# Performance work log

Hardware: AMD Instinct MI355X
Metric: run time of the kernel (lower is better)

Reference implementation:

```python
import jax, jax.numpy as jnp
import numpy as np
import math

N_PATHS = 2048
N_STEPS = 512
N_FWD = 40
N_FACTORS = 3
H = 0.1
ALPHA = H - 0.5            # fBM kernel exponent
BETA_SABR = 0.5
SHIFT = 0.02
DT = 1.0 / N_STEPS
GAMMA_CONST = math.gamma(H + 0.5)
BETA_DECAY = 0.05


def setup_inputs() -> dict:
    key = jax.random.key(0)
    tenors = np.linspace(0.0, 10.0, N_FWD + 1)
    T = tenors[:-1]
    tau = np.diff(tenors).astype(np.float32)
    F0 = np.full(N_FWD, 0.02, dtype=np.float32)
    # alphas = base normal vols / |F0+shift|^beta  (as in __init__)
    base_vols = np.full(N_FWD, 0.006)
    eta_F0 = np.abs(F0 + SHIFT) ** BETA_SABR
    alphas = (base_vols / eta_F0).astype(np.float32)
    rhos = np.full(N_FWD, -0.3, dtype=np.float32)
    nus = np.full(N_FWD, 0.5, dtype=np.float32)
    # PCA loadings from exponential spatial correlation (as in __init__)
    corr = np.exp(-BETA_DECAY * np.abs(T[:, None] - T[None, :]))
    evals, evecs = np.linalg.eigh(corr)
    idx = np.argsort(evals)[::-1][:N_FACTORS]
    L = evecs[:, idx] * np.sqrt(np.clip(evals[idx], 0.0, None))[None, :]
    L = L / np.sqrt((L ** 2).sum(axis=1, keepdims=True))
    Lam = np.triu(L @ L.T, 1).astype(np.float32)
    # Brownian increments, pre-scaled by sqrt(dt) (replaces Sobol+icdf draw)
    dz = jax.random.normal(key, (N_PATHS, N_STEPS, N_FACTORS + 1), dtype=jnp.float32) * float(np.sqrt(DT))
    return {
        "dz_all": dz,
        "F0": jnp.asarray(F0),
        "alphas": jnp.asarray(alphas),
        "rhos": jnp.asarray(rhos),
        "nus": jnp.asarray(nus),
        "tau": jnp.asarray(tau),
        "loadings": jnp.asarray(L.astype(np.float32)),
        "Lambda_upper": jnp.asarray(Lam),
    }


def reference(dz_all, F0, alphas, rhos, nus, tau, loadings, Lambda_upper):
    n_paths, n_steps, _ = dz_all.shape
    dtype = dz_all.dtype
    # --- hybrid-scheme Volterra / fBM kernel [n_steps, n_steps] ---
    idx = jnp.arange(n_steps)
    k = jnp.maximum(idx[:, None] - idx[None, :] + 1, 0).astype(dtype)
    # with b_eval='optimal', riemann == exact weights, so the where(k<=kappa) is identity
    exact_w = (k ** (ALPHA + 1.0) - jnp.maximum(k - 1.0, 0.0) ** (ALPHA + 1.0)) / (ALPHA + 1.0)
    kernel = jnp.where(idx[:, None] >= idx[None, :], exact_w * (DT ** ALPHA) / GAMMA_CONST, 0.0)
    # variance compensator [N, n_steps]
    var_comp = 0.5 * (nus ** 2)[:, None] * jnp.sum(kernel ** 2, axis=1)[None, :] * DT
    # --- correlated Brownian drivers and fBM via kernel convolution ---
    wr = jnp.einsum('psf,nf->psn', dz_all[..., :N_FACTORS], loadings)          # [P,S,N]
    fbm4 = jnp.einsum('ts,psd->ptd', kernel, dz_all)                            # [P,S,4]
    fbm_curve = jnp.einsum('ptf,nf->ptn', fbm4[..., :N_FACTORS], loadings)      # [P,S,N]
    fbm = rhos * fbm_curve + jnp.sqrt(1.0 - rhos ** 2) * fbm4[..., -1:]
    unit_vols = jnp.exp(nus * fbm - var_comp.T[None])                            # [P,S,N]
    v2_dt = unit_vols ** 2 * DT
    # --- frozen-drift forward dynamics ---
    eta_f0 = jnp.abs(F0 + SHIFT) ** BETA_SABR
    vol_scale = alphas * eta_f0
    omega_0 = tau * vol_scale / (1.0 + tau * F0)
    mu_0 = -vol_scale * (Lambda_upper @ omega_0)
    dF = mu_0 * v2_dt + wr * (unit_vols * vol_scale)
    F_path = F0 + jnp.cumsum(dF, axis=1)                                         # [P,S,N]
    return jnp.concatenate([jnp.broadcast_to(F0, (n_paths, 1, F0.shape[0])), F_path], axis=1)
```

## Files before the change

kernel.cpp:

```cpp
#include <hip/hip_runtime.h>
#include <math.h>

#define NS 512
#define NF 40
#define ROWS_OUT 513
#define DTC (1.0f / 512.0f)
#define PLANE 512

typedef short bf16x8 __attribute__((ext_vector_type(8)));
typedef float f32x4 __attribute__((ext_vector_type(4)));

#define W_BYTES_NEEDED (1344u * 4u + 512u * 512u * 2u)

__device__ __forceinline__ unsigned short f2bf(float x) {
    unsigned int u = __float_as_uint(x);
    return (unsigned short)((u + 0x7FFFu + ((u >> 16) & 1u)) >> 16);
}

__global__ __launch_bounds__(64) void const_kernel(
    const float* __restrict__ F0, const float* __restrict__ alphas,
    const float* __restrict__ rhos, const float* __restrict__ nus,
    const float* __restrict__ tau, const float* __restrict__ L,
    const float* __restrict__ Lam, float* __restrict__ ws)
{
    __shared__ double wd[NS];
    __shared__ float omega0[NF];
    __shared__ float vs_s[NF];
    int n = threadIdx.x;
    {
        const double g06 = 1.4891922488128171;
        const double dta = pow(512.0, 0.4);
        #pragma unroll
        for (int k = 0; k < 8; ++k) {
            int m = n * 8 + k;
            double wv = (pow((double)m + 1.0, 0.6) - pow((double)m, 0.6)) * (1.0 / 0.6) * dta / g06;
            wd[m] = wv;
            ws[m] = (float)wv;
        }
    }
    if (n < NF) {
        float f0 = F0[n];
        float vs = alphas[n] * sqrtf(fabsf(f0 + 0.02f));
        vs_s[n] = vs;
        omega0[n] = tau[n] * vs / (1.0f + tau[n] * f0);
    }
    __syncthreads();
    if (n == 0) {
        double acc = 0.0;
        for (int m = 0; m < NS; ++m) { acc += wd[m] * wd[m]; ws[NS + m] = (float)acc; }
    }
    if (n < NF) {
        float s = 0.0f;
        for (int j = 0; j < NF; ++j) s += Lam[n * NF + j] * omega0[j];
        float vs = vs_s[n];
        float mu0 = -vs * s;
        float rho = rhos[n], nu = nus[n];
        float* c = ws + 1024 + n * 8;
        c[0] = vs * L[n * 3 + 0];
        c[1] = vs * L[n * 3 + 1];
        c[2] = vs * L[n * 3 + 2];
        c[3] = nu * rho / fmaxf(vs, 1e-30f);
        c[4] = nu * sqrtf(fmaxf(1.0f - rho * rho, 0.0f));
        c[5] = 0.5f * nu * nu * DTC;
        c[6] = mu0 * DTC;
        c[7] = F0[n];
    }
}

__global__ __launch_bounds__(128) void toeplitz_kernel(float* __restrict__ ws)
{
    int t = blockIdx.x;
    int s0 = threadIdx.x * 4;
    ushort4 v;
    v.x = (s0 + 0 <= t) ? f2bf(ws[t - s0 - 0]) : (unsigned short)0;
    v.y = (s0 + 1 <= t) ? f2bf(ws[t - s0 - 1]) : (unsigned short)0;
    v.z = (s0 + 2 <= t) ? f2bf(ws[t - s0 - 2]) : (unsigned short)0;
    v.w = (s0 + 3 <= t) ? f2bf(ws[t - s0 - 3]) : (unsigned short)0;
    ushort4* W = (ushort4*)((unsigned short*)(ws + 1344) + (size_t)t * 512);
    W[threadIdx.x] = v;
}

template<int CTRL, int RM>
__device__ __forceinline__ float dpp_add(float v) {
    int t = __builtin_amdgcn_update_dpp(0, __float_as_int(v), CTRL, RM, 0xf, true);
    return v + __int_as_float(t);
}
__device__ __forceinline__ float wave_iscan(float v) {
    v = dpp_add<0x111, 0xf>(v);
    v = dpp_add<0x112, 0xf>(v);
    v = dpp_add<0x114, 0xf>(v);
    v = dpp_add<0x118, 0xf>(v);
    v = dpp_add<0x142, 0xa>(v);
    v = dpp_add<0x143, 0xc>(v);
    return v;
}

__device__ __forceinline__ void fma4(float4& acc, float c, const float4& v) {
    acc.x = fmaf(c, v.x, acc.x);
    acc.y = fmaf(c, v.y, acc.y);
    acc.z = fmaf(c, v.z, acc.z);
    acc.w = fmaf(c, v.w, acc.w);
}

__global__ __launch_bounds__(256, 8) void path_kernel_mfma(
    const float* __restrict__ dz, const float* __restrict__ ws,
    float* __restrict__ out)
{
    __shared__ float planes[NS * 4];
    __shared__ float ustage[64 * 41];

    int tid = threadIdx.x;
    int lane = tid & 63;
    int wv = __builtin_amdgcn_readfirstlane(tid >> 6);
    int p = blockIdx.x;
    const float4* dzg = (const float4*)dz + (size_t)p * NS;

    unsigned short* dzb = (unsigned short*)ustage;
    {
        int k2 = tid * 2;
        float4 da = dzg[k2], db = dzg[k2 + 1];
        unsigned int* d32 = (unsigned int*)dzb;
        d32[0 * 256 + tid] = (unsigned int)f2bf(da.x) | ((unsigned int)f2bf(db.x) << 16);
        d32[1 * 256 + tid] = (unsigned int)f2bf(da.y) | ((unsigned int)f2bf(db.y) << 16);
        d32[2 * 256 + tid] = (unsigned int)f2bf(da.z) | ((unsigned int)f2bf(db.z) << 16);
        d32[3 * 256 + tid] = (unsigned int)f2bf(da.w) | ((unsigned int)f2bf(db.w) << 16);
    }
    __syncthreads();

    {
        const unsigned short* W = (const unsigned short*)(ws + 1344);
        int arow = lane & 15, ksub = lane >> 4;
        f32x4 acc[8];
        #pragma unroll
        for (int j = 0; j < 8; ++j) acc[j] = (f32x4){0.f, 0.f, 0.f, 0.f};
        const unsigned short* bbase = dzb + (lane & 3) * 512 + ksub * 8;
        #pragma unroll 1
        for (int k = 0; k < 16; ++k) {
            bf16x8 bf = *(const bf16x8*)(bbase + k * 32);
            #pragma unroll
            for (int j = 0; j < 8; ++j) {
                int m = wv + 4 * j;
                if (k <= ((16 * m + 15) >> 5)) {
                    bf16x8 af = *(const bf16x8*)(W + (size_t)(16 * m + arow) * NS + k * 32 + ksub * 8);
                    acc[j] = __builtin_amdgcn_mfma_f32_16x16x32_bf16(af, bf, acc[j], 0, 0, 0);
                }
            }
        }
        if (arow < 4) {
            #pragma unroll
            for (int j = 0; j < 8; ++j) {
                int m = wv + 4 * j;
                #pragma unroll
                for (int r = 0; r < 4; ++r)
                    planes[(16 * m + ksub * 4 + r) * 4 + arow] = acc[j][r];
            }
        }
    }

    float carry[10];
    #pragma unroll
    for (int j = 0; j < 10; ++j) carry[j] = 0.0f;

    float* outP = out + (size_t)p * (ROWS_OUT * NF);
    if (tid < NF) outP[tid] = ws[1024 + tid * 8 + 7];

    __syncthreads();

    float* chunk = ustage;
    const float* cwg = ws + NS;
    const float4* planes4 = (const float4*)planes;
    for (int cix = 0; cix < 8; ++cix) {
        int t = cix * 64 + lane;
        float cw = cwg[t];
        float4 f4 = planes4[t];
        float fx = f4.x, fy = f4.y, fz = f4.z, fw = f4.w;
        float4 d = dzg[t];
        #pragma unroll
        for (int j = 0; j < 10; ++j) {
            int n = wv * 10 + j;
            const float* c = ws + 1024 + n * 8;
            float cC0 = c[0], cC1 = c[1], cC2 = c[2], q = c[3];
            float cA3 = c[4], ca = c[5], cm0 = c[6], f0 = c[7];
            float dotf = fx * cC0 + fy * cC1 + fz * cC2;
            float arg = fmaf(q, dotf, fmaf(cA3, fw, -ca * cw));
            float uv = __expf(arg);
            float dotc = d.x * cC0 + d.y * cC1 + d.z * cC2;
            float dF = uv * fmaf(cm0, uv, dotc);
            float v = wave_iscan(dF) + carry[j];
            carry[j] = __int_as_float(__builtin_amdgcn_readlane(__float_as_int(v), 63));
            chunk[lane * 41 + n] = v + f0;
        }
        __syncthreads();
        float* o = outP + NF + cix * (64 * NF);
        #pragma unroll
        for (int k = 0; k < 10; ++k) {
            int f = tid + k * 256;
            __builtin_nontemporal_store(chunk[f + f / 40], o + f);
        }
        __syncthreads();
    }
}

__global__ __launch_bounds__(256, 8) void path_kernel(
    const float* __restrict__ dz, const float* __restrict__ ws,
    float* __restrict__ out)
{
    __shared__ float planes[4 * PLANE];
    __shared__ float ustage[64 * 41];

    int tid = threadIdx.x;
    int lane = tid & 63;
    int wv = __builtin_amdgcn_readfirstlane(tid >> 6);
    int p = blockIdx.x;
    const float4* dzg = (const float4*)dz + (size_t)p * NS;

    float* wp = ustage;
    for (int i = tid; i < 768; i += 256) wp[i] = (i < 256) ? 0.0f : ws[i - 256];
    __syncthreads();

    {
        int role = (wv + p) & 3;
        int half = role >> 1;
        int seg  = role & 1;
        int i = half * 64 + lane;
        int span = half ? 64 : 32;
        int g0 = seg * span, g1 = g0 + span;
        const float4* wp4 = (const float4*)wp;
        float4 a0 = make_float4(0.f, 0.f, 0.f, 0.f);
        float4 a1 = a0, a2 = a0, a3 = a0;
        #pragma unroll 2
        for (int g = g0; g < g1; ++g) {
            float4 d0 = dzg[4 * g + 0];
            float4 d1 = dzg[4 * g + 1];
            float4 d2 = dzg[4 * g + 2];
            float4 d3 = dzg[4 * g + 3];
            float4 lo = wp4[63 + i - g];
            float4 hi = wp4[64 + i - g];
            fma4(a0, hi.x, d0); fma4(a1, hi.y, d0); fma4(a2, hi.z, d0); fma4(a3, hi.w, d0);
            fma4(a0, lo.w, d1); fma4(a1, hi.x, d1); fma4(a2, hi.y, d1); fma4(a3, hi.z, d1);
            fma4(a0, lo.z, d2); fma4(a1, lo.w, d2); fma4(a2, hi.x, d2); fma4(a3, hi.y, d2);
            fma4(a0, lo.y, d3); fma4(a1, lo.z, d3); fma4(a2, lo.w, d3); fma4(a3, hi.x, d3);
        }
        if (seg == 1) {
            ((float4*)(planes + 0 * PLANE))[i] = make_float4(a0.x, a1.x, a2.x, a3.x);
            ((float4*)(planes + 1 * PLANE))[i] = make_float4(a0.y, a1.y, a2.y, a3.y);
            ((float4*)(planes + 2 * PLANE))[i] = make_float4(a0.z, a1.z, a2.z, a3.z);
            ((float4*)(planes + 3 * PLANE))[i] = make_float4(a0.w, a1.w, a2.w, a3.w);
        }
        __syncthreads();
        if (seg == 0) {
            float4* q0 = &((float4*)(planes + 0 * PLANE))[i];
            float4* q1 = &((float4*)(planes + 1 * PLANE))[i];
            float4* q2 = &((float4*)(planes + 2 * PLANE))[i];
            float4* q3 = &((float4*)(planes + 3 * PLANE))[i];
            float4 c0 = *q0, c1 = *q1, c2 = *q2, c3 = *q3;
            c0.x += a0.x; c0.y += a1.x; c0.z += a2.x; c0.w += a3.x;
            c1.x += a0.y; c1.y += a1.y; c1.z += a2.y; c1.w += a3.y;
            c2.x += a0.z; c2.y += a1.z; c2.z += a2.z; c2.w += a3.z;
            c3.x += a0.w; c3.y += a1.w; c3.z += a2.w; c3.w += a3.w;
            *q0 = c0; *q1 = c1; *q2 = c2; *q3 = c3;
        }
        __syncthreads();
    }

    float carry[10];
    #pragma unroll
    for (int j = 0; j < 10; ++j) carry[j] = 0.0f;

    float* outP = out + (size_t)p * (ROWS_OUT * NF);
    if (tid < NF) outP[tid] = ws[1024 + tid * 8 + 7];

    float* chunk = ustage;
    const float* cwg = ws + NS;
    for (int cix = 0; cix < 8; ++cix) {
        int t = cix * 64 + lane;
        float cw = cwg[t];
        float fx = planes[t], fy = planes[PLANE + t];
        float fz = planes[2 * PLANE + t], fw = planes[3 * PLANE + t];
        float4 d = dzg[t];
        #pragma unroll
        for (int j = 0; j < 10; ++j) {
            int n = wv * 10 + j;
            const float* c = ws + 1024 + n * 8;
            float cC0 = c[0], cC1 = c[1], cC2 = c[2], q = c[3];
            float cA3 = c[4], ca = c[5], cm0 = c[6], f0 = c[7];
            float dotf = fx * cC0 + fy * cC1 + fz * cC2;
            float arg = fmaf(q, dotf, fmaf(cA3, fw, -ca * cw));
            float uv = __expf(arg);
            float dotc = d.x * cC0 + d.y * cC1 + d.z * cC2;
            float dF = uv * fmaf(cm0, uv, dotc);
            float v = wave_iscan(dF) + carry[j];
            carry[j] = __int_as_float(__builtin_amdgcn_readlane(__float_as_int(v), 63));
            chunk[lane * 41 + n] = v + f0;
        }
        __syncthreads();
        float* o = outP + NF + cix * (64 * NF);
        #pragma unroll
        for (int k = 0; k < 10; ++k) {
            int f = tid + k * 256;
            __builtin_nontemporal_store(chunk[f + f / 40], o + f);
        }
        __syncthreads();
    }
}

extern "C" void kernel_launch(void* const* d_in, const int* in_sizes, int n_in,
                              void* d_out, int out_size, void* d_ws, size_t ws_size,
                              hipStream_t stream) {
    const float* dz   = (const float*)d_in[0];
    const float* F0   = (const float*)d_in[1];
    const float* alph = (const float*)d_in[2];
    const float* rhos = (const float*)d_in[3];
    const float* nus  = (const float*)d_in[4];
    const float* tau  = (const float*)d_in[5];
    const float* L    = (const float*)d_in[6];
    const float* Lam  = (const float*)d_in[7];
    float* ws = (float*)d_ws;
    float* out = (float*)d_out;

    int n_paths = in_sizes[0] / (NS * 4);

    const_kernel<<<1, 64, 0, stream>>>(F0, alph, rhos, nus, tau, L, Lam, ws);
    if (ws_size >= (size_t)W_BYTES_NEEDED) {
        toeplitz_kernel<<<512, 128, 0, stream>>>(ws);
        path_kernel_mfma<<<n_paths, 256, 0, stream>>>(dz, ws, out);
    } else {
        path_kernel<<<n_paths, 256, 0, stream>>>(dz, ws, out);
    }
}
```

Baseline: 280.5 us.

## Split Toeplitz MFMA into separate batched kernel processing four paths per block

```diff
diff --git a/kernel.cpp b/kernel.cpp
--- a/kernel.cpp
+++ b/kernel.cpp
@@ -6,11 +6,12 @@
 #define ROWS_OUT 513
 #define DTC (1.0f / 512.0f)
 #define PLANE 512
+#define WOFF 132416
+#define LOG2E 1.4426950408889634f
 
 typedef short bf16x8 __attribute__((ext_vector_type(8)));
 typedef float f32x4 __attribute__((ext_vector_type(4)));
 
-#define W_BYTES_NEEDED (1344u * 4u + 512u * 512u * 2u)
 
 __device__ __forceinline__ unsigned short f2bf(float x) {
     unsigned int u = __float_as_uint(x);
@@ -59,9 +60,9 @@
         c[0] = vs * L[n * 3 + 0];
         c[1] = vs * L[n * 3 + 1];
         c[2] = vs * L[n * 3 + 2];
-        c[3] = nu * rho / fmaxf(vs, 1e-30f);
-        c[4] = nu * sqrtf(fmaxf(1.0f - rho * rho, 0.0f));
-        c[5] = 0.5f * nu * nu * DTC;
+        c[3] = (nu * rho / fmaxf(vs, 1e-30f)) * LOG2E;
+        c[4] = (nu * sqrtf(fmaxf(1.0f - rho * rho, 0.0f))) * LOG2E;
+        c[5] = (0.5f * nu * nu * DTC) * LOG2E;
         c[6] = mu0 * DTC;
         c[7] = F0[n];
     }
@@ -102,60 +103,70 @@
     acc.w = fmaf(c, v.w, acc.w);
 }
 
-__global__ __launch_bounds__(256, 8) void path_kernel_mfma(
+__global__ __launch_bounds__(256, 4) void gemmB_kernel(
+    const float* __restrict__ dz, float* __restrict__ ws)
+{
+    __shared__ unsigned short dzb[16 * 520];
+    int tid = threadIdx.x;
+    int lane = tid & 63;
+    int wv = __builtin_amdgcn_readfirstlane(tid >> 6);
+    int p0 = blockIdx.x * 4;
+
+    {
+        const float4* dzg = (const float4*)dz + (size_t)(p0 + wv) * NS;
+        unsigned int* d32 = (unsigned int*)dzb;
+        #pragma unroll
+        for (int it = 0; it < 4; ++it) {
+            int k2 = it * 128 + lane * 2;
+            float4 da = dzg[k2], db = dzg[k2 + 1];
+            int o = it * 64 + lane;
+            d32[(wv * 4 + 0) * 260 + o] = (unsigned int)f2bf(da.x) | ((unsigned int)f2bf(db.x) << 16);
+            d32[(wv * 4 + 1) * 260 + o] = (unsigned int)f2bf(da.y) | ((unsigned int)f2bf(db.y) << 16);
+            d32[(wv * 4 + 2) * 260 + o] = (unsigned int)f2bf(da.z) | ((unsigned int)f2bf(db.z) << 16);
+            d32[(wv * 4 + 3) * 260 + o] = (unsigned int)f2bf(da.w) | ((unsigned int)f2bf(db.w) << 16);
+        }
+    }
+    __syncthreads();
+
+    const unsigned short* W = (const unsigned short*)(ws + 1344);
+    int col = lane & 15, ksub = lane >> 4;
+    f32x4 acc[8];
+    #pragma unroll
+    for (int j = 0; j < 8; ++j) acc[j] = (f32x4){0.f, 0.f, 0.f, 0.f};
+    const unsigned short* bbase = dzb + col * 520 + ksub * 8;
+    #pragma unroll 1
+    for (int k = 0; k < 16; ++k) {
+        bf16x8 bfv = *(const bf16x8*)(bbase + k * 32);
+        #pragma unroll
+        for (int j = 0; j < 8; ++j) {
+            int m = wv + 4 * j;
+            if (k <= ((16 * m + 15) >> 5)) {
+                bf16x8 af = *(const bf16x8*)(W + (size_t)(16 * m + col) * NS + k * 32 + ksub * 8);
+                acc[j] = __builtin_amdgcn_mfma_f32_16x16x32_bf16(af, bfv, acc[j], 0, 0, 0);
+            }
+        }
+    }
+    float* pg = ws + WOFF + ((size_t)(p0 + (col >> 2)) * 4 + (col & 3)) * NS;
+    #pragma unroll
+    for (int j = 0; j < 8; ++j) {
+        int t0 = 16 * (wv + 4 * j) + ksub * 4;
+        *(float4*)(pg + t0) = make_float4(acc[j][0], acc[j][1], acc[j][2], acc[j][3]);
+    }
+}
+
+__global__ __launch_bounds__(256, 8) void pathCD_kernel(
     const float* __restrict__ dz, const float* __restrict__ ws,
     float* __restrict__ out)
 {
-    __shared__ float planes[NS * 4];
-    __shared__ float ustage[64 * 41];
+    __shared__ float chunk[64 * 41];
 
     int tid = threadIdx.x;
     int lane = tid & 63;
     int wv = __builtin_amdgcn_readfirstlane(tid >> 6);
     int p = blockIdx.x;
     const float4* dzg = (const float4*)dz + (size_t)p * NS;
-
-    unsigned short* dzb = (unsigned short*)ustage;
-    {
-        int k2 = tid * 2;
-        float4 da = dzg[k2], db = dzg[k2 + 1];
-        unsigned int* d32 = (unsigned int*)dzb;
-        d32[0 * 256 + tid] = (unsigned int)f2bf(da.x) | ((unsigned int)f2bf(db.x) << 16);
-        d32[1 * 256 + tid] = (unsigned int)f2bf(da.y) | ((unsigned int)f2bf(db.y) << 16);
-        d32[2 * 256 + tid] = (unsigned int)f2bf(da.z) | ((unsigned int)f2bf(db.z) << 16);
-        d32[3 * 256 + tid] = (unsigned int)f2bf(da.w) | ((unsigned int)f2bf(db.w) << 16);
-    }
-    __syncthreads();
-
-    {
-        const unsigned short* W = (const unsigned short*)(ws + 1344);
-        int arow = lane & 15, ksub = lane >> 4;
-        f32x4 acc[8];
-        #pragma unroll
-        for (int j = 0; j < 8; ++j) acc[j] = (f32x4){0.f, 0.f, 0.f, 0.f};
-        const unsigned short* bbase = dzb + (lane & 3) * 512 + ksub * 8;
-        #pragma unroll 1
-        for (int k = 0; k < 16; ++k) {
-            bf16x8 bf = *(const bf16x8*)(bbase + k * 32);
-            #pragma unroll
-            for (int j = 0; j < 8; ++j) {
-                int m = wv + 4 * j;
-                if (k <= ((16 * m + 15) >> 5)) {
-                    bf16x8 af = *(const bf16x8*)(W + (size_t)(16 * m + arow) * NS + k * 32 + ksub * 8);
-                    acc[j] = __builtin_amdgcn_mfma_f32_16x16x32_bf16(af, bf, acc[j], 0, 0, 0);
-                }
-            }
-        }
-        if (arow < 4) {
-            #pragma unroll
-            for (int j = 0; j < 8; ++j) {
-                int m = wv + 4 * j;
-                #pragma unroll
-                for (int r = 0; r < 4; ++r)
-                    planes[(16 * m + ksub * 4 + r) * 4 + arow] = acc[j][r];
-            }
-        }
-    }
+    const float* pg = ws + WOFF + (size_t)p * 4 * NS;
+    const float* cwg = ws + NS;
 
     float carry[10];
     #pragma unroll
@@ -164,16 +175,10 @@
     float* outP = out + (size_t)p * (ROWS_OUT * NF);
     if (tid < NF) outP[tid] = ws[1024 + tid * 8 + 7];
 
-    __syncthreads();
-
-    float* chunk = ustage;
-    const float* cwg = ws + NS;
-    const float4* planes4 = (const float4*)planes;
     for (int cix = 0; cix < 8; ++cix) {
         int t = cix * 64 + lane;
         float cw = cwg[t];
-        float4 f4 = planes4[t];
-        float fx = f4.x, fy = f4.y, fz = f4.z, fw = f4.w;
+        float fx = pg[t], fy = pg[NS + t], fz = pg[2 * NS + t], fw = pg[3 * NS + t];
         float4 d = dzg[t];
         #pragma unroll
         for (int j = 0; j < 10; ++j) {
@@ -183,7 +188,7 @@
             float cA3 = c[4], ca = c[5], cm0 = c[6], f0 = c[7];
             float dotf = fx * cC0 + fy * cC1 + fz * cC2;
             float arg = fmaf(q, dotf, fmaf(cA3, fw, -ca * cw));
-            float uv = __expf(arg);
+            float uv = exp2f(arg);
             float dotc = d.x * cC0 + d.y * cC1 + d.z * cC2;
             float dF = uv * fmaf(cm0, uv, dotc);
             float v = wave_iscan(dF) + carry[j];
@@ -286,7 +291,7 @@
             float cA3 = c[4], ca = c[5], cm0 = c[6], f0 = c[7];
             float dotf = fx * cC0 + fy * cC1 + fz * cC2;
             float arg = fmaf(q, dotf, fmaf(cA3, fw, -ca * cw));
-            float uv = __expf(arg);
+            float uv = exp2f(arg);
             float dotc = d.x * cC0 + d.y * cC1 + d.z * cC2;
             float dF = uv * fmaf(cm0, uv, dotc);
             float v = wave_iscan(dF) + carry[j];
@@ -319,11 +324,13 @@
     float* out = (float*)d_out;
 
     int n_paths = in_sizes[0] / (NS * 4);
+    size_t full_bytes = ((size_t)WOFF + (size_t)n_paths * 4 * NS) * 4;
 
     const_kernel<<<1, 64, 0, stream>>>(F0, alph, rhos, nus, tau, L, Lam, ws);
-    if (ws_size >= (size_t)W_BYTES_NEEDED) {
+    if (ws_size >= full_bytes && (n_paths & 3) == 0) {
         toeplitz_kernel<<<512, 128, 0, stream>>>(ws);
-        path_kernel_mfma<<<n_paths, 256, 0, stream>>>(dz, ws, out);
+        gemmB_kernel<<<n_paths / 4, 256, 0, stream>>>(dz, ws);
+        pathCD_kernel<<<n_paths, 256, 0, stream>>>(dz, ws, out);
     } else {
         path_kernel<<<n_paths, 256, 0, stream>>>(dz, ws, out);
     }
```

After: 248.3 us. 11.5% less time.
